# Performance work log

Hardware: AMD Instinct MI355X
Metric: run time of the kernel (lower is better)

The kernel has to match this reference:

```python
import jax, jax.numpy as jnp
import numpy as np

N_NODES = 100000

def setup_inputs() -> dict:
    key = jax.random.key(0)
    k1, k2, k3 = jax.random.split(key, 3)
    x = jax.random.normal(k1, (N_NODES, 64), dtype=jnp.float32)
    edge_index = jax.random.randint(k2, (2, 1600000), 0, N_NODES, dtype=jnp.int64)
    edge_weights = jax.random.uniform(k3, (1600000,), dtype=jnp.float32)
    weight = jnp.ones((1,), dtype=jnp.float32)  # MyConv.weight, reset to 1
    return {"x": x, "edge_index": edge_index, "edge_weights": edge_weights, "weight": weight}

def reference(x, edge_index, edge_weights, weight):
    src = edge_index[0]  # x_j (source nodes, messages flow source->target)
    dst = edge_index[1]  # aggregation target i
    # message: edge_weight * x_j ; aggregate: scatter-add at dst
    msgs = edge_weights[:, None] * x[src]              # [E, D]
    agg = jax.ops.segment_sum(msgs, dst, num_segments=N_NODES)  # [N, D]
    # conv1: x + weight * aggregate, then relu (Encoder only applies conv1)
    return jax.nn.relu(x + weight * agg)
```

## Files before the change

### kernel.cpp

```cpp
#include <hip/hip_runtime.h>

constexpr int N_NODES = 100000;
constexpr int D       = 64;
constexpr int N_EDGES = 1600000;
constexpr int OUT_N4  = N_NODES * D / 4;

constexpr int NPB   = 128;
constexpr int NBUCK = (N_NODES + NPB - 1) / NPB;
constexpr int BCAP  = 2560;
constexpr int CPAD  = 32;
constexpr int PTHREADS = 1024;
constexpr int EPT   = 4;
constexpr int CHUNK = PTHREADS * EPT;
constexpr int PB    = (N_EDGES + CHUNK - 1) / CHUNK;

__global__ void detect_kernel(const unsigned long long* __restrict__ ei,
                              int* __restrict__ flag) {
    if (blockIdx.x == 0 && threadIdx.x == 0) {
        int is64 = 1;
#pragma unroll
        for (int i = 0; i < 8; ++i)
            if (ei[i] >= (unsigned long long)N_NODES) is64 = 0;
        *flag = is64;
    }
}

__device__ __forceinline__ int load_idx(const void* ei_raw, int flag, long long pos) {
    if (flag) return (int)((const long long*)ei_raw)[pos];
    return ((const int*)ei_raw)[pos];
}

__device__ __forceinline__ unsigned short bf16rne(float f) {
    unsigned u = __float_as_uint(f);
    unsigned r = (u + 0x7fffu + ((u >> 16) & 1u)) >> 16;
    return (unsigned short)r;
}

__global__ void prep_kernel(const float4* __restrict__ x4,
                            ushort4* __restrict__ x16v,
                            int* __restrict__ cursor) {
    int i = blockIdx.x * blockDim.x + threadIdx.x;
    int stride = gridDim.x * blockDim.x;
    for (int j = i; j < NBUCK * CPAD; j += stride) cursor[j] = 0;
    for (; i < OUT_N4; i += stride) {
        float4 v = x4[i];
        ushort4 o;
        o.x = bf16rne(v.x); o.y = bf16rne(v.y);
        o.z = bf16rne(v.z); o.w = bf16rne(v.w);
        x16v[i] = o;
    }
}

__global__ __launch_bounds__(PTHREADS) void part_kernel(
        const void* __restrict__ ei_raw,
        const float* __restrict__ ew,
        const int* __restrict__ flag,
        int* __restrict__ cursor,
        int2* __restrict__ slots) {
    __shared__ int  hist[NBUCK];
    __shared__ int  localbase[NBUCK];
    __shared__ int  runbase[NBUCK];
    __shared__ int  fill[NBUCK];
    __shared__ int  wsum[16];
    __shared__ int  tot;
    __shared__ int2 srt[CHUNK];
    __shared__ unsigned short aux[CHUNK];

    int tid  = threadIdx.x;
    int wv   = tid >> 6;
    int lane = tid & 63;
    for (int t = tid; t < NBUCK; t += PTHREADS) { hist[t] = 0; fill[t] = 0; }
    __syncthreads();

    int f = *flag;
    long long base = (long long)blockIdx.x * CHUNK;

    int  rb[EPT];
    int2 rrec[EPT];
#pragma unroll
    for (int it = 0; it < EPT; ++it) {
        long long e = base + it * PTHREADS + tid;
        if (e < N_EDGES) {
            int src = load_idx(ei_raw, f, e);
            int dst = load_idx(ei_raw, f, (long long)N_EDGES + e);
            int b = dst >> 7;
            rb[it] = b;
            rrec[it].x = (src << 7) | (dst & (NPB - 1));
            rrec[it].y = __float_as_int(ew[e]);
            atomicAdd(&hist[b], 1);
        } else {
            rb[it] = -1;
        }
    }
    __syncthreads();

    int h = (tid < NBUCK) ? hist[tid] : 0;
    int v = h;
#pragma unroll
    for (int off = 1; off < 64; off <<= 1) {
        int u = __shfl_up(v, off, 64);
        if (lane >= off) v += u;
    }
    if (lane == 63) wsum[wv] = v;
    __syncthreads();
    if (wv == 0 && lane < 16) {
        int s = wsum[lane];
        int t2 = s;
#pragma unroll
        for (int off = 1; off < 16; off <<= 1) {
            int u = __shfl_up(t2, off, 64);
            if (lane >= off) t2 += u;
        }
        wsum[lane] = t2 - s;
        if (lane == 15) tot = t2;
    }
    __syncthreads();
    if (tid < NBUCK) {
        localbase[tid] = (v - h) + wsum[wv];
        int c = hist[tid];
        runbase[tid] = (c > 0) ? atomicAdd(&cursor[tid * CPAD], c) : 0;
    }
    __syncthreads();

#pragma unroll
    for (int it = 0; it < EPT; ++it) {
        int b = rb[it];
        if (b >= 0) {
            int p = localbase[b] + atomicAdd(&fill[b], 1);
            srt[p] = rrec[it];
            aux[p] = (unsigned short)b;
        }
    }
    __syncthreads();

    int total = tot;
    for (int i = tid; i < total; i += PTHREADS) {
        int b = aux[i];
        int g = runbase[b] + (i - localbase[b]);
        if (g < BCAP) slots[(long long)b * BCAP + g] = srt[i];
    }
}

__global__ __launch_bounds__(PTHREADS) void sg_kernel(
        const unsigned short* __restrict__ x16,
        const int* __restrict__ cursor,
        const int2* __restrict__ slots,
        const float* __restrict__ weight,
        float* __restrict__ out) {
    __shared__ int  hist[NPB];
    __shared__ int  nbeg[NPB];
    __shared__ int  fill[NPB];
    __shared__ int2 raw[BCAP];
    __shared__ int2 srt[BCAP];

    int tid  = threadIdx.x;
    int wv   = tid >> 6;
    int lane = tid & 63;
    int b    = blockIdx.x;

    if (tid < NPB) { hist[tid] = 0; fill[tid] = 0; }
    __syncthreads();

    int cnt = cursor[b * CPAD];
    if (cnt > BCAP) cnt = BCAP;
    const int2* sb = slots + (long long)b * BCAP;

    for (int i = tid; i < cnt; i += PTHREADS) {
        int2 r = sb[i];
        raw[i] = r;
        atomicAdd(&hist[r.x & (NPB - 1)], 1);
    }
    __syncthreads();

    if (wv == 0) {
        int h0 = hist[2 * lane];
        int h1 = hist[2 * lane + 1];
        int s  = h0 + h1;
        int v  = s;
#pragma unroll
        for (int off = 1; off < 64; off <<= 1) {
            int u = __shfl_up(v, off, 64);
            if (lane >= off) v += u;
        }
        int excl = v - s;
        nbeg[2 * lane]     = excl;
        nbeg[2 * lane + 1] = excl + h0;
    }
    __syncthreads();

    for (int i = tid; i < cnt; i += PTHREADS) {
        int2 r = raw[i];
        int dl = r.x & (NPB - 1);
        int pos = nbeg[dl] + atomicAdd(&fill[dl], 1);
        srt[pos] = r;
    }
    __syncthreads();

    int rg = lane >> 3;
    int dg = lane & 7;
    float W = weight[0];

    for (int dl = wv * 8; dl < wv * 8 + 8; ++dl) {
        int node = b * NPB + dl;
        if (node >= N_NODES) continue;
        int nb = nbeg[dl];
        int nc = hist[dl];

        float acc[8];
#pragma unroll
        for (int j = 0; j < 8; ++j) acc[j] = 0.f;

        for (int k = 0; k < nc; k += 16) {
            int iA = k + rg;
            int iB = iA + 8;
            int2 rA = srt[nb + (iA < nc ? iA : 0)];
            int2 rB = srt[nb + (iB < nc ? iB : 0)];
            float wA = (iA < nc) ? __int_as_float(rA.y) : 0.f;
            float wB = (iB < nc) ? __int_as_float(rB.y) : 0.f;
            uint4 xa = *(const uint4*)(x16 + (rA.x >> 7) * D + dg * 8);
            uint4 xb = *(const uint4*)(x16 + (rB.x >> 7) * D + dg * 8);
#pragma unroll
            for (int j = 0; j < 4; ++j) {
                unsigned ua = ((const unsigned*)&xa)[j];
                acc[2 * j]     += wA * __uint_as_float(ua << 16);
                acc[2 * j + 1] += wA * __uint_as_float(ua & 0xffff0000u);
            }
#pragma unroll
            for (int j = 0; j < 4; ++j) {
                unsigned ub = ((const unsigned*)&xb)[j];
                acc[2 * j]     += wB * __uint_as_float(ub << 16);
                acc[2 * j + 1] += wB * __uint_as_float(ub & 0xffff0000u);
            }
        }

#pragma unroll
        for (int j = 0; j < 8; ++j) {
            acc[j] += __shfl_xor(acc[j], 8, 64);
            acc[j] += __shfl_xor(acc[j], 16, 64);
            acc[j] += __shfl_xor(acc[j], 32, 64);
        }

        if (rg == 0) {
            uint4 xs = *(const uint4*)(x16 + node * D + dg * 8);
            float o[8];
#pragma unroll
            for (int j = 0; j < 4; ++j) {
                unsigned us = ((const unsigned*)&xs)[j];
                o[2 * j]     = fmaxf(__uint_as_float(us << 16)         + W * acc[2 * j],     0.f);
                o[2 * j + 1] = fmaxf(__uint_as_float(us & 0xffff0000u) + W * acc[2 * j + 1], 0.f);
            }
            float4* po = (float4*)(out + node * D + dg * 8);
            po[0] = make_float4(o[0], o[1], o[2], o[3]);
            po[1] = make_float4(o[4], o[5], o[6], o[7]);
        }
    }
}

__global__ void init_out_kernel(const float4* __restrict__ x4,
                                float4* __restrict__ out4) {
    int i = blockIdx.x * blockDim.x + threadIdx.x;
    int stride = gridDim.x * blockDim.x;
    for (; i < OUT_N4; i += stride) out4[i] = x4[i];
}

__global__ __launch_bounds__(256) void scatter_atomic_kernel(
        const float* __restrict__ x,
        const void* __restrict__ ei_raw,
        const float* __restrict__ ew,
        const float* __restrict__ weight,
        const int* __restrict__ flag,
        float* __restrict__ out) {
    long long gid = (long long)blockIdx.x * blockDim.x + threadIdx.x;
    int e = (int)(gid >> 6);
    int d = (int)(gid & 63);
    if (e >= N_EDGES) return;
    int f = *flag;
    int src = load_idx(ei_raw, f, e);
    int dst = load_idx(ei_raw, f, (long long)N_EDGES + e);
    float w = weight[0] * ew[e];
    atomicAdd(&out[dst * D + d], w * x[src * D + d]);
}

__global__ void relu_kernel(float4* __restrict__ out4) {
    int i = blockIdx.x * blockDim.x + threadIdx.x;
    int stride = gridDim.x * blockDim.x;
    for (; i < OUT_N4; i += stride) {
        float4 v = out4[i];
        v.x = fmaxf(v.x, 0.0f);
        v.y = fmaxf(v.y, 0.0f);
        v.z = fmaxf(v.z, 0.0f);
        v.w = fmaxf(v.w, 0.0f);
        out4[i] = v;
    }
}

extern "C" void kernel_launch(void* const* d_in, const int* in_sizes, int n_in,
                              void* d_out, int out_size, void* d_ws, size_t ws_size,
                              hipStream_t stream) {
    const float* x      = (const float*)d_in[0];
    const void*  ei     = d_in[1];
    const float* ew     = (const float*)d_in[2];
    const float* weight = (const float*)d_in[3];
    float* out = (float*)d_out;

    char* w = (char*)d_ws;
    auto align256 = [](size_t v) { return (v + 255) & ~(size_t)255; };

    size_t off = 0;
    int* flag = (int*)(w + off);        off = align256(off + 4);
    int* cursor = (int*)(w + off);      off = align256(off + (size_t)NBUCK * CPAD * 4);
    unsigned short* x16 = (unsigned short*)(w + off);
                                        off = align256(off + (size_t)N_NODES * D * 2);
    int2* slots = (int2*)(w + off);     off = align256(off + (size_t)NBUCK * BCAP * 8);
    size_t needed = off;

    detect_kernel<<<1, 64, 0, stream>>>((const unsigned long long*)ei, flag);

    if (ws_size >= needed) {
        prep_kernel<<<2048, 256, 0, stream>>>((const float4*)x, (ushort4*)x16, cursor);
        part_kernel<<<PB, PTHREADS, 0, stream>>>(ei, ew, flag, cursor, slots);
        sg_kernel<<<NBUCK, PTHREADS, 0, stream>>>(x16, cursor, slots, weight, out);
    } else {
        init_out_kernel<<<2048, 256, 0, stream>>>((const float4*)x, (float4*)out);
        long long total = (long long)N_EDGES * 64;
        scatter_atomic_kernel<<<(int)((total + 255) / 256), 256, 0, stream>>>(
            x, ei, ew, weight, flag, out);
        relu_kernel<<<2048, 256, 0, stream>>>((float4*)out);
    }
}
```

Measured before the change: 89.13 us.

## Halve sg_kernel block size, drop raw LDS staging, gather two nodes per wave

The gather kernel now runs with 512 threads per block instead of 1024, so each wave handles 16 destination nodes, processed two at a time with four gathered rows in flight per iteration. The raw shared-memory staging buffer is removed and the bucket's slot records are read from global memory twice, once for the histogram and once for the sort, which frees LDS for more resident blocks. The intent is more memory-level parallelism and occupancy in the gather. The cost is extra global reads and wasted lanes when the two paired nodes have uneven edge counts.

```diff
diff --git a/kernel.cpp b/kernel.cpp
--- a/kernel.cpp
+++ b/kernel.cpp
@@ -13,6 +13,7 @@
 constexpr int EPT   = 4;
 constexpr int CHUNK = PTHREADS * EPT;
 constexpr int PB    = (N_EDGES + CHUNK - 1) / CHUNK;
+constexpr int SGT   = 512;
 
 __global__ void detect_kernel(const unsigned long long* __restrict__ ei,
                               int* __restrict__ flag) {
@@ -141,7 +142,7 @@
     }
 }
 
-__global__ __launch_bounds__(PTHREADS) void sg_kernel(
+__global__ __launch_bounds__(SGT) void sg_kernel(
         const unsigned short* __restrict__ x16,
         const int* __restrict__ cursor,
         const int2* __restrict__ slots,
@@ -150,7 +151,6 @@
     __shared__ int  hist[NPB];
     __shared__ int  nbeg[NPB];
     __shared__ int  fill[NPB];
-    __shared__ int2 raw[BCAP];
     __shared__ int2 srt[BCAP];
 
     int tid  = threadIdx.x;
@@ -165,11 +165,8 @@
     if (cnt > BCAP) cnt = BCAP;
     const int2* sb = slots + (long long)b * BCAP;
 
-    for (int i = tid; i < cnt; i += PTHREADS) {
-        int2 r = sb[i];
-        raw[i] = r;
-        atomicAdd(&hist[r.x & (NPB - 1)], 1);
-    }
+    for (int i = tid; i < cnt; i += SGT)
+        atomicAdd(&hist[sb[i].x & (NPB - 1)], 1);
     __syncthreads();
 
     if (wv == 0) {
@@ -188,8 +185,8 @@
     }
     __syncthreads();
 
-    for (int i = tid; i < cnt; i += PTHREADS) {
-        int2 r = raw[i];
+    for (int i = tid; i < cnt; i += SGT) {
+        int2 r = sb[i];
         int dl = r.x & (NPB - 1);
         int pos = nbeg[dl] + atomicAdd(&fill[dl], 1);
         srt[pos] = r;
@@ -200,54 +197,75 @@
     int dg = lane & 7;
     float W = weight[0];
 
-    for (int dl = wv * 8; dl < wv * 8 + 8; ++dl) {
-        int node = b * NPB + dl;
-        if (node >= N_NODES) continue;
-        int nb = nbeg[dl];
-        int nc = hist[dl];
-
-        float acc[8];
-#pragma unroll
-        for (int j = 0; j < 8; ++j) acc[j] = 0.f;
-
-        for (int k = 0; k < nc; k += 16) {
-            int iA = k + rg;
-            int iB = iA + 8;
-            int2 rA = srt[nb + (iA < nc ? iA : 0)];
-            int2 rB = srt[nb + (iB < nc ? iB : 0)];
-            float wA = (iA < nc) ? __int_as_float(rA.y) : 0.f;
-            float wB = (iB < nc) ? __int_as_float(rB.y) : 0.f;
-            uint4 xa = *(const uint4*)(x16 + (rA.x >> 7) * D + dg * 8);
-            uint4 xb = *(const uint4*)(x16 + (rB.x >> 7) * D + dg * 8);
+    for (int dl0 = wv * 16; dl0 < wv * 16 + 16; dl0 += 2) {
+        int nodeA = b * NPB + dl0;
+        int nodeB = nodeA + 1;
+        bool vA = (nodeA < N_NODES);
+        bool vB = (nodeB < N_NODES);
+        if (!vA) break;
+
+        int begA = nbeg[dl0],     ncA = hist[dl0];
+        int begB = nbeg[dl0 + 1], ncB = vB ? hist[dl0 + 1] : 0;
+
+        float accA[8], accB[8];
+#pragma unroll
+        for (int j = 0; j < 8; ++j) { accA[j] = 0.f; accB[j] = 0.f; }
+
+        int kmax = ncA > ncB ? ncA : ncB;
+        for (int k = 0; k < kmax; k += 16) {
+            int a1 = k + rg,  a2 = a1 + 8;
+            int2 rA1 = srt[begA + (a1 < ncA ? a1 : 0)];
+            int2 rA2 = srt[begA + (a2 < ncA ? a2 : 0)];
+            int2 rB1 = srt[begB + (a1 < ncB ? a1 : 0)];
+            int2 rB2 = srt[begB + (a2 < ncB ? a2 : 0)];
+            float wA1 = (a1 < ncA) ? __int_as_float(rA1.y) : 0.f;
+            float wA2 = (a2 < ncA) ? __int_as_float(rA2.y) : 0.f;
+            float wB1 = (a1 < ncB) ? __int_as_float(rB1.y) : 0.f;
+            float wB2 = (a2 < ncB) ? __int_as_float(rB2.y) : 0.f;
+            uint4 xa1 = *(const uint4*)(x16 + (rA1.x >> 7) * D + dg * 8);
+            uint4 xa2 = *(const uint4*)(x16 + (rA2.x >> 7) * D + dg * 8);
+            uint4 xb1 = *(const uint4*)(x16 + (rB1.x >> 7) * D + dg * 8);
+            uint4 xb2 = *(const uint4*)(x16 + (rB2.x >> 7) * D + dg * 8);
 #pragma unroll
             for (int j = 0; j < 4; ++j) {
-                unsigned ua = ((const unsigned*)&xa)[j];
-                acc[2 * j]     += wA * __uint_as_float(ua << 16);
-                acc[2 * j + 1] += wA * __uint_as_float(ua & 0xffff0000u);
+                unsigned u1 = ((const unsigned*)&xa1)[j];
+                unsigned u2 = ((const unsigned*)&xa2)[j];
+                accA[2 * j]     += wA1 * __uint_as_float(u1 << 16)
+                                 + wA2 * __uint_as_float(u2 << 16);
+                accA[2 * j + 1] += wA1 * __uint_as_float(u1 & 0xffff0000u)
+                                 + wA2 * __uint_as_float(u2 & 0xffff0000u);
             }
 #pragma unroll
             for (int j = 0; j < 4; ++j) {
-                unsigned ub = ((const unsigned*)&xb)[j];
-                acc[2 * j]     += wB * __uint_as_float(ub << 16);
-                acc[2 * j + 1] += wB * __uint_as_float(ub & 0xffff0000u);
+                unsigned u1 = ((const unsigned*)&xb1)[j];
+                unsigned u2 = ((const unsigned*)&xb2)[j];
+                accB[2 * j]     += wB1 * __uint_as_float(u1 << 16)
+                                 + wB2 * __uint_as_float(u2 << 16);
+                accB[2 * j + 1] += wB1 * __uint_as_float(u1 & 0xffff0000u)
+                                 + wB2 * __uint_as_float(u2 & 0xffff0000u);
             }
         }
 
 #pragma unroll
         for (int j = 0; j < 8; ++j) {
-            acc[j] += __shfl_xor(acc[j], 8, 64);
-            acc[j] += __shfl_xor(acc[j], 16, 64);
-            acc[j] += __shfl_xor(acc[j], 32, 64);
-        }
-
-        if (rg == 0) {
+            accA[j] += __shfl_xor(accA[j], 8, 64);
+            accA[j] += __shfl_xor(accA[j], 16, 64);
+            accA[j] += __shfl_xor(accA[j], 32, 64);
+            accB[j] += __shfl_xor(accB[j], 8, 64);
+            accB[j] += __shfl_xor(accB[j], 16, 64);
+            accB[j] += __shfl_xor(accB[j], 32, 64);
+        }
+
+        if (rg == 0 || (rg == 1 && vB)) {
+            int   node = (rg == 0) ? nodeA : nodeB;
+            float* accp = (rg == 0) ? accA : accB;
             uint4 xs = *(const uint4*)(x16 + node * D + dg * 8);
             float o[8];
 #pragma unroll
             for (int j = 0; j < 4; ++j) {
                 unsigned us = ((const unsigned*)&xs)[j];
-                o[2 * j]     = fmaxf(__uint_as_float(us << 16)         + W * acc[2 * j],     0.f);
-                o[2 * j + 1] = fmaxf(__uint_as_float(us & 0xffff0000u) + W * acc[2 * j + 1], 0.f);
+                o[2 * j]     = fmaxf(__uint_as_float(us << 16)         + W * accp[2 * j],     0.f);
+                o[2 * j + 1] = fmaxf(__uint_as_float(us & 0xffff0000u) + W * accp[2 * j + 1], 0.f);
             }
             float4* po = (float4*)(out + node * D + dg * 8);
             po[0] = make_float4(o[0], o[1], o[2], o[3]);
@@ -319,7 +337,7 @@
     if (ws_size >= needed) {
         prep_kernel<<<2048, 256, 0, stream>>>((const float4*)x, (ushort4*)x16, cursor);
         part_kernel<<<PB, PTHREADS, 0, stream>>>(ei, ew, flag, cursor, slots);
-        sg_kernel<<<NBUCK, PTHREADS, 0, stream>>>(x16, cursor, slots, weight, out);
+        sg_kernel<<<NBUCK, SGT, 0, stream>>>(x16, cursor, slots, weight, out);
     } else {
         init_out_kernel<<<2048, 256, 0, stream>>>((const float4*)x, (float4*)out);
         long long total = (long long)N_EDGES * 64;
```

Result: no change. 89.90 us (+0.9%).
